# Performance work log

Hardware: AMD Instinct MI355X
Metric: run time of the kernel (lower is better)

The kernel has to match this reference:

```python
import jax, jax.numpy as jnp
import numpy as np

N, G, C, H, S = 16384, 100, 10, 32, 10  # batch, nb_genes, nb_chrom, hidden, signature
BN_EPS = 1e-5
SLOPE = 0.2


def setup_inputs() -> dict:
    key = jax.random.key(0)
    k = jax.random.split(key, 7)
    x = jax.random.randint(k[0], (N, G), 0, 3)                      # categorical genotype per gene
    emb = jax.random.normal(k[1], (G, 3, H), dtype=jnp.float32)      # per-gene entity embedding tables
    gene_att = jax.random.normal(k[2], (C, H), dtype=jnp.float32)    # GeneAttentionLayer attention matrix
    chrom_att = jax.random.normal(k[3], (1, H), dtype=jnp.float32)   # ChromAttentionLayer attention vector
    W = jax.random.normal(k[4], (H, S), dtype=jnp.float32) * 0.1     # linear layer weight
    b = jnp.zeros((S,), dtype=jnp.float32)                           # linear layer bias
    bn_gamma = jnp.ones((S,), dtype=jnp.float32)
    bn_beta = jnp.zeros((S,), dtype=jnp.float32)
    return {"x": x, "emb": emb, "gene_att": gene_att, "chrom_att": chrom_att,
            "W": W, "b": b, "bn_gamma": bn_gamma, "bn_beta": bn_beta}


def reference(x, emb, gene_att, chrom_att, W, b, bn_gamma, bn_beta):
    nb_genes, nb_chrom, hid = emb.shape[0], gene_att.shape[0], emb.shape[2]
    genes_per_chrom = nb_genes // nb_chrom
    # chrom composition matrix: comp[i, j] = 1 iff gene j belongs to chromosome i (contiguous blocks)
    comp = (jnp.arange(nb_genes) // genes_per_chrom == jnp.arange(nb_chrom)[:, None]).astype(emb.dtype)

    # --- entity embedding: h[n, g] = emb[g, x[n, g]]  -> (N, G, H)
    h = emb[jnp.arange(nb_genes)[None, :], x]

    # --- GeneAttentionLayer (avoids the dense (N, C, G, H) intermediate of the torch code)
    att = jnp.einsum('ch,ngh->ncg', gene_att, h) * comp[None]        # (N, C, G)
    mask = (att != 0).astype(h.dtype)                                # matches att.bool().byte()
    a = jnp.exp(jax.nn.leaky_relu(att, SLOPE)) * mask
    a = a / jnp.maximum(a.sum(axis=2, keepdims=True), 1e-10)
    chrom = jnp.einsum('ncg,ngh->nch', a, h)                         # (N, C, H) chromosome embeddings
    chrom = jax.nn.relu(chrom)                                       # dropout p=0 -> identity

    # --- ChromAttentionLayer
    catt = jnp.einsum('h,nch->nc', chrom_att[0], chrom)              # (N, C)
    ca = jnp.exp(jax.nn.leaky_relu(catt, SLOPE))
    ca = ca / ca.sum(axis=1, keepdims=True)
    g = jnp.einsum('nc,nch->nh', ca, chrom)                          # (N, H)
    g = jax.nn.relu(g)

    # --- linear + batch norm (training-mode batch statistics, biased variance as in torch BN)
    y = g @ W + b                                                    # (N, S)
    mu = y.mean(axis=0)
    var = ((y - mu) ** 2).mean(axis=0)
    return (y - mu) / jnp.sqrt(var + BN_EPS) * bn_gamma + bn_beta
```

## Files before the change

### kernel.cpp

```cpp
#include <hip/hip_runtime.h>
#include <hip/hip_fp16.h>

#define NROWS 16384
#define NG 100
#define NC 10
#define NH 32
#define NS 10
#define GPC 10
#define SLOPE 0.2f
#define BN_EPS 1e-5f

#define EPADH 36
#define RPB 32
#define BLOCK_A 512
#define NB (NROWS / RPB)


template<bool SLOTS>
__global__ __launch_bounds__(BLOCK_A, 4) void gga_main(
    const int* __restrict__ x, const float* __restrict__ emb,
    const float* __restrict__ gene_att, const float* __restrict__ chrom_att,
    const float* __restrict__ W, const float* __restrict__ b,
    float* __restrict__ y, float* __restrict__ P)
{
    __shared__ __half embL[300 * EPADH];
    __shared__ float eL[300];
    __shared__ float WTL[NS * NH];
    __shared__ float bL[NS];
    __shared__ unsigned xpL[RPB * 8];
    __shared__ float sAcc[2 * NS];

    const int t = threadIdx.x;
    const int n0 = blockIdx.x * RPB;

    for (int i = t; i < 2400; i += BLOCK_A) {
        float4 v = reinterpret_cast<const float4*>(emb)[i];
        int f = i << 2;
        int row = f >> 5, h = f & 31;
        __half2 lo = __floats2half2_rn(v.x, v.y);
        __half2 hi = __floats2half2_rn(v.z, v.w);
        uint2 u;
        u.x = __builtin_bit_cast(unsigned, lo);
        u.y = __builtin_bit_cast(unsigned, hi);
        *reinterpret_cast<uint2*>(&embL[row * EPADH + h]) = u;
    }
    for (int i = t; i < NH * NS; i += BLOCK_A) {
        int s = i >> 5, h = i & 31;
        WTL[i] = W[h * NS + s];
    }
    if (t < NS) bL[t] = b[t];
    if (t < 2 * NS) sAcc[t] = 0.f;
    if (t < 300) {
        const int g = t / 3;
        const float* ga = gene_att + (g / GPC) * NH;
        const float* e = emb + t * NH;
        float s = 0.f;
#pragma unroll
        for (int k = 0; k < NH; k += 4) {
            float4 ev = *reinterpret_cast<const float4*>(e + k);
            float4 gv = *reinterpret_cast<const float4*>(ga + k);
            s = fmaf(gv.x, ev.x, s); s = fmaf(gv.y, ev.y, s);
            s = fmaf(gv.z, ev.z, s); s = fmaf(gv.w, ev.w, s);
        }
        const float lk = s > 0.f ? s : SLOPE * s;
        eL[t] = (s != 0.f) ? __expf(lk) : 0.f;
    }
    if (t < 256) {
        const int r = t >> 3, w = t & 7;
        unsigned pw = 0u;
        if (w < 7) {
            const int4* p = reinterpret_cast<const int4*>(x + (n0 + r) * NG + w * 16);
            const int nv = (w < 6) ? 4 : 1;
#pragma unroll
            for (int i = 0; i < 4; ++i) {
                if (i < nv) {
                    int4 v = p[i];
                    pw |= ((unsigned)v.x & 3u) << (i * 8 + 0);
                    pw |= ((unsigned)v.y & 3u) << (i * 8 + 2);
                    pw |= ((unsigned)v.z & 3u) << (i * 8 + 4);
                    pw |= ((unsigned)v.w & 3u) << (i * 8 + 6);
                }
            }
        }
        xpL[r * 8 + w] = pw;
    }
    __syncthreads();

    const int lr = t >> 4;
    const int o = t & 15;
    const int n = n0 + lr;

    const float2 ca = reinterpret_cast<const float2*>(chrom_att)[o];

    const uint4 pa = *reinterpret_cast<const uint4*>(&xpL[lr * 8]);
    const uint4 pb = *reinterpret_cast<const uint4*>(&xpL[lr * 8 + 4]);
    const unsigned pk[8] = {pa.x, pa.y, pa.z, pa.w, pb.x, pb.y, pb.z, pb.w};

    float2 num = {0.f, 0.f};
    float den = 0.f;

#pragma unroll
    for (int c = 0; c < NC; ++c) {
        float e[GPC];
        float2 hf[GPC];
#pragma unroll
        for (int gp = 0; gp < GPC; ++gp) {
            const int g = c * GPC + gp;
            const unsigned xg = (pk[g >> 4] >> ((g & 15) * 2)) & 3u;
            const int r3 = g * 3 + (int)xg;
            e[gp] = eL[r3];
            __half2 hh = *reinterpret_cast<const __half2*>(&embL[r3 * EPADH + o * 2]);
            hf[gp] = __half22float2(hh);
        }
        float suma = 0.f;
#pragma unroll
        for (int gp = 0; gp < GPC; ++gp) suma += e[gp];
        const float inv = 1.f / fmaxf(suma, 1e-10f);

        float2 ch = {0.f, 0.f};
#pragma unroll
        for (int gp = 0; gp < GPC; ++gp) {
            ch.x = fmaf(e[gp], hf[gp].x, ch.x);
            ch.y = fmaf(e[gp], hf[gp].y, ch.y);
        }
        ch.x = fmaxf(ch.x, 0.f);
        ch.y = fmaxf(ch.y, 0.f);

        float pc = ch.x * ca.x + ch.y * ca.y;
        pc += __shfl_xor(pc, 1);
        pc += __shfl_xor(pc, 2);
        pc += __shfl_xor(pc, 4);
        pc += __shfl_xor(pc, 8);
        pc *= inv;
        const float lc = pc > 0.f ? pc : SLOPE * pc;
        const float ec = __expf(lc);
        const float w = ec * inv;

        num.x = fmaf(w, ch.x, num.x);
        num.y = fmaf(w, ch.y, num.y);
        den += ec;
    }

    const float invd = 1.f / den;
    const float g0 = fmaxf(num.x * invd, 0.f);
    const float g1 = fmaxf(num.y * invd, 0.f);

    float ys[NS];
#pragma unroll
    for (int s = 0; s < NS; ++s) {
        const float2 wv = *reinterpret_cast<const float2*>(&WTL[s * NH + o * 2]);
        float p = g0 * wv.x + g1 * wv.y;
        p += __shfl_xor(p, 1);
        p += __shfl_xor(p, 2);
        p += __shfl_xor(p, 4);
        p += __shfl_xor(p, 8);
        ys[s] = p + bL[s];
    }

    if (o == 0) {
        float2* yp = reinterpret_cast<float2*>(y + n * NS);
#pragma unroll
        for (int s2 = 0; s2 < 5; ++s2) yp[s2] = make_float2(ys[2 * s2], ys[2 * s2 + 1]);
    }

#pragma unroll
    for (int s = 0; s < NS; ++s) {
        float v = ys[s];
        float v2 = ys[s] * ys[s];
        v += __shfl_xor(v, 16);  v2 += __shfl_xor(v2, 16);
        v += __shfl_xor(v, 32);  v2 += __shfl_xor(v2, 32);
        if ((t & 63) == 0) {
            atomicAdd(&sAcc[s], v);
            atomicAdd(&sAcc[NS + s], v2);
        }
    }
    __syncthreads();
    if (t < 2 * NS) {
        if (SLOTS) P[t * NB + blockIdx.x] = sAcc[t];
        else       atomicAdd(&P[t], sAcc[t]);
    }
}

template<bool SLOTS>
__global__ __launch_bounds__(256) void gga_bn(
    float* __restrict__ out, const float* __restrict__ P,
    const float* __restrict__ gamma, const float* __restrict__ beta)
{
    __shared__ float red[2 * NS * 8];
    __shared__ float scL[NS], shL[NS];
    const int t = threadIdx.x;

    if (SLOTS) {
        if (t < 2 * NS * 8) {
            const int k = t >> 3, c = t & 7;
            const float4* p4 = reinterpret_cast<const float4*>(P + k * NB + c * 64);
            float s = 0.f;
#pragma unroll
            for (int i = 0; i < 16; ++i) {
                float4 v = p4[i];
                s += v.x + v.y + v.z + v.w;
            }
            red[t] = s;
        }
        __syncthreads();
    }
    if (t < NS) {
        float sm, sq;
        if (SLOTS) {
            sm = 0.f; sq = 0.f;
#pragma unroll
            for (int c = 0; c < 8; ++c) {
                sm += red[t * 8 + c];
                sq += red[(NS + t) * 8 + c];
            }
        } else {
            sm = P[t]; sq = P[NS + t];
        }
        const float mu = sm * (1.f / NROWS);
        float var = sq * (1.f / NROWS) - mu * mu;
        var = fmaxf(var, 0.f);
        const float r = rsqrtf(var + BN_EPS);
        scL[t] = gamma[t] * r;
        shL[t] = beta[t] - mu * scL[t];
    }
    __syncthreads();

    const int i4 = (blockIdx.x * 256 + t) * 4;
    float4 v = *reinterpret_cast<const float4*>(out + i4);
    const int s0 = i4 % NS;
    const int s1 = (s0 + 1) % NS, s2 = (s0 + 2) % NS, s3 = (s0 + 3) % NS;
    v.x = fmaf(v.x, scL[s0], shL[s0]);
    v.y = fmaf(v.y, scL[s1], shL[s1]);
    v.z = fmaf(v.z, scL[s2], shL[s2]);
    v.w = fmaf(v.w, scL[s3], shL[s3]);
    *reinterpret_cast<float4*>(out + i4) = v;
}

extern "C" void kernel_launch(void* const* d_in, const int* in_sizes, int n_in,
                              void* d_out, int out_size, void* d_ws, size_t ws_size,
                              hipStream_t stream) {
    const int*   x         = (const int*)d_in[0];
    const float* emb       = (const float*)d_in[1];
    const float* gene_att  = (const float*)d_in[2];
    const float* chrom_att = (const float*)d_in[3];
    const float* W         = (const float*)d_in[4];
    const float* b         = (const float*)d_in[5];
    const float* bn_gamma  = (const float*)d_in[6];
    const float* bn_beta   = (const float*)d_in[7];

    float* y = (float*)d_out;
    float* P = (float*)d_ws;

    if (ws_size >= (size_t)(2 * NS * NB * sizeof(float))) {
        gga_main<true><<<NB, BLOCK_A, 0, stream>>>(
            x, emb, gene_att, chrom_att, W, b, y, P);
        gga_bn<true><<<(NROWS * NS) / (256 * 4), 256, 0, stream>>>(
            y, P, bn_gamma, bn_beta);
    } else {
        hipMemsetAsync(P, 0, 2 * NS * sizeof(float), stream);
        gga_main<false><<<NB, BLOCK_A, 0, stream>>>(
            x, emb, gene_att, chrom_att, W, b, y, P);
        gga_bn<false><<<(NROWS * NS) / (256 * 4), 256, 0, stream>>>(
            y, P, bn_gamma, bn_beta);
    }
}
```

Before: 26.52 us.

## Halve threads per row, use DPP reductions, stripe global BN stat atomics

Each row is now handled by 8 lanes instead of 16, each lane covering 4 hidden dims with 64-bit LDS loads, and the block size drops to 256. Cross-lane sums use DPP row operations instead of ds_swizzle/shuffles. The per-block partial-sum slots and shared-memory atomics are replaced by global atomics spread over 8 stripes, with a memset before launch, which simplifies the BN kernel's reduction. The trade-offs are more global atomic contention and an extra memset launch, in exchange for fewer reduction instructions and less per-block overhead.

```diff
diff --git a/kernel.cpp b/kernel.cpp
--- a/kernel.cpp
+++ b/kernel.cpp
@@ -12,12 +12,23 @@
 
 #define EPADH 36
 #define RPB 32
-#define BLOCK_A 512
+#define BLOCK_A 256
 #define NB (NROWS / RPB)
 
-
-template<bool SLOTS>
-__global__ __launch_bounds__(BLOCK_A, 4) void gga_main(
+template<int CTRL>
+__device__ __forceinline__ float dpp_add(float v) {
+    int x = __builtin_bit_cast(int, v);
+    int y = __builtin_amdgcn_update_dpp(0, x, CTRL, 0xF, 0xF, true);
+    return v + __builtin_bit_cast(float, y);
+}
+__device__ __forceinline__ float row8_allreduce(float v) {
+    v = dpp_add<0xB1>(v);
+    v = dpp_add<0x4E>(v);
+    v = dpp_add<0x141>(v);
+    return v;
+}
+
+__global__ __launch_bounds__(BLOCK_A, 2) void gga_main(
     const int* __restrict__ x, const float* __restrict__ emb,
     const float* __restrict__ gene_att, const float* __restrict__ chrom_att,
     const float* __restrict__ W, const float* __restrict__ b,
@@ -28,7 +39,6 @@
     __shared__ float WTL[NS * NH];
     __shared__ float bL[NS];
     __shared__ unsigned xpL[RPB * 8];
-    __shared__ float sAcc[2 * NS];
 
     const int t = threadIdx.x;
     const int n0 = blockIdx.x * RPB;
@@ -49,11 +59,10 @@
         WTL[i] = W[h * NS + s];
     }
     if (t < NS) bL[t] = b[t];
-    if (t < 2 * NS) sAcc[t] = 0.f;
-    if (t < 300) {
-        const int g = t / 3;
+    for (int i = t; i < 300; i += BLOCK_A) {
+        const int g = i / 3;
         const float* ga = gene_att + (g / GPC) * NH;
-        const float* e = emb + t * NH;
+        const float* e = emb + i * NH;
         float s = 0.f;
 #pragma unroll
         for (int k = 0; k < NH; k += 4) {
@@ -63,9 +72,9 @@
             s = fmaf(gv.z, ev.z, s); s = fmaf(gv.w, ev.w, s);
         }
         const float lk = s > 0.f ? s : SLOPE * s;
-        eL[t] = (s != 0.f) ? __expf(lk) : 0.f;
-    }
-    if (t < 256) {
+        eL[i] = (s != 0.f) ? __expf(lk) : 0.f;
+    }
+    {
         const int r = t >> 3, w = t & 7;
         unsigned pw = 0u;
         if (w < 7) {
@@ -86,74 +95,73 @@
     }
     __syncthreads();
 
-    const int lr = t >> 4;
-    const int o = t & 15;
+    const int lr = t >> 3;
+    const int o = t & 7;
     const int n = n0 + lr;
 
-    const float2 ca = reinterpret_cast<const float2*>(chrom_att)[o];
+    const float4 ca = reinterpret_cast<const float4*>(chrom_att)[o];
 
     const uint4 pa = *reinterpret_cast<const uint4*>(&xpL[lr * 8]);
     const uint4 pb = *reinterpret_cast<const uint4*>(&xpL[lr * 8 + 4]);
     const unsigned pk[8] = {pa.x, pa.y, pa.z, pa.w, pb.x, pb.y, pb.z, pb.w};
 
-    float2 num = {0.f, 0.f};
+    float4 num = {0.f, 0.f, 0.f, 0.f};
     float den = 0.f;
 
 #pragma unroll
     for (int c = 0; c < NC; ++c) {
         float e[GPC];
-        float2 hf[GPC];
+        uint2 hu[GPC];
 #pragma unroll
         for (int gp = 0; gp < GPC; ++gp) {
             const int g = c * GPC + gp;
             const unsigned xg = (pk[g >> 4] >> ((g & 15) * 2)) & 3u;
             const int r3 = g * 3 + (int)xg;
             e[gp] = eL[r3];
-            __half2 hh = *reinterpret_cast<const __half2*>(&embL[r3 * EPADH + o * 2]);
-            hf[gp] = __half22float2(hh);
+            hu[gp] = *reinterpret_cast<const uint2*>(&embL[r3 * EPADH + o * 4]);
         }
         float suma = 0.f;
 #pragma unroll
         for (int gp = 0; gp < GPC; ++gp) suma += e[gp];
         const float inv = 1.f / fmaxf(suma, 1e-10f);
 
-        float2 ch = {0.f, 0.f};
+        float4 ch = {0.f, 0.f, 0.f, 0.f};
 #pragma unroll
         for (int gp = 0; gp < GPC; ++gp) {
-            ch.x = fmaf(e[gp], hf[gp].x, ch.x);
-            ch.y = fmaf(e[gp], hf[gp].y, ch.y);
-        }
-        ch.x = fmaxf(ch.x, 0.f);
-        ch.y = fmaxf(ch.y, 0.f);
-
-        float pc = ch.x * ca.x + ch.y * ca.y;
-        pc += __shfl_xor(pc, 1);
-        pc += __shfl_xor(pc, 2);
-        pc += __shfl_xor(pc, 4);
-        pc += __shfl_xor(pc, 8);
+            float2 a = __half22float2(__builtin_bit_cast(__half2, hu[gp].x));
+            float2 d = __half22float2(__builtin_bit_cast(__half2, hu[gp].y));
+            ch.x = fmaf(e[gp], a.x, ch.x);
+            ch.y = fmaf(e[gp], a.y, ch.y);
+            ch.z = fmaf(e[gp], d.x, ch.z);
+            ch.w = fmaf(e[gp], d.y, ch.w);
+        }
+        ch.x = fmaxf(ch.x, 0.f); ch.y = fmaxf(ch.y, 0.f);
+        ch.z = fmaxf(ch.z, 0.f); ch.w = fmaxf(ch.w, 0.f);
+
+        float pc = ch.x * ca.x + ch.y * ca.y + ch.z * ca.z + ch.w * ca.w;
+        pc = row8_allreduce(pc);
         pc *= inv;
         const float lc = pc > 0.f ? pc : SLOPE * pc;
         const float ec = __expf(lc);
         const float w = ec * inv;
 
-        num.x = fmaf(w, ch.x, num.x);
-        num.y = fmaf(w, ch.y, num.y);
+        num.x = fmaf(w, ch.x, num.x); num.y = fmaf(w, ch.y, num.y);
+        num.z = fmaf(w, ch.z, num.z); num.w = fmaf(w, ch.w, num.w);
         den += ec;
     }
 
     const float invd = 1.f / den;
     const float g0 = fmaxf(num.x * invd, 0.f);
     const float g1 = fmaxf(num.y * invd, 0.f);
+    const float g2 = fmaxf(num.z * invd, 0.f);
+    const float g3 = fmaxf(num.w * invd, 0.f);
 
     float ys[NS];
 #pragma unroll
     for (int s = 0; s < NS; ++s) {
-        const float2 wv = *reinterpret_cast<const float2*>(&WTL[s * NH + o * 2]);
-        float p = g0 * wv.x + g1 * wv.y;
-        p += __shfl_xor(p, 1);
-        p += __shfl_xor(p, 2);
-        p += __shfl_xor(p, 4);
-        p += __shfl_xor(p, 8);
+        const float4 wv = *reinterpret_cast<const float4*>(&WTL[s * NH + o * 4]);
+        float p = g0 * wv.x + g1 * wv.y + g2 * wv.z + g3 * wv.w;
+        p = row8_allreduce(p);
         ys[s] = p + bL[s];
     }
 
@@ -163,58 +171,34 @@
         for (int s2 = 0; s2 < 5; ++s2) yp[s2] = make_float2(ys[2 * s2], ys[2 * s2 + 1]);
     }
 
+    const int kstripe = (int)(blockIdx.x & 7);
 #pragma unroll
     for (int s = 0; s < NS; ++s) {
-        float v = ys[s];
+        float v  = ys[s];
         float v2 = ys[s] * ys[s];
-        v += __shfl_xor(v, 16);  v2 += __shfl_xor(v2, 16);
-        v += __shfl_xor(v, 32);  v2 += __shfl_xor(v2, 32);
+        v  = dpp_add<0x128>(v);
+        v2 = dpp_add<0x128>(v2);
+        v  += __shfl_xor(v, 16);  v2 += __shfl_xor(v2, 16);
+        v  += __shfl_xor(v, 32);  v2 += __shfl_xor(v2, 32);
         if ((t & 63) == 0) {
-            atomicAdd(&sAcc[s], v);
-            atomicAdd(&sAcc[NS + s], v2);
-        }
-    }
-    __syncthreads();
-    if (t < 2 * NS) {
-        if (SLOTS) P[t * NB + blockIdx.x] = sAcc[t];
-        else       atomicAdd(&P[t], sAcc[t]);
-    }
-}
-
-template<bool SLOTS>
+            atomicAdd(&P[kstripe * 64 + s],      v);
+            atomicAdd(&P[kstripe * 64 + 32 + s], v2);
+        }
+    }
+}
+
 __global__ __launch_bounds__(256) void gga_bn(
     float* __restrict__ out, const float* __restrict__ P,
     const float* __restrict__ gamma, const float* __restrict__ beta)
 {
-    __shared__ float red[2 * NS * 8];
     __shared__ float scL[NS], shL[NS];
     const int t = threadIdx.x;
-
-    if (SLOTS) {
-        if (t < 2 * NS * 8) {
-            const int k = t >> 3, c = t & 7;
-            const float4* p4 = reinterpret_cast<const float4*>(P + k * NB + c * 64);
-            float s = 0.f;
-#pragma unroll
-            for (int i = 0; i < 16; ++i) {
-                float4 v = p4[i];
-                s += v.x + v.y + v.z + v.w;
-            }
-            red[t] = s;
-        }
-        __syncthreads();
-    }
     if (t < NS) {
-        float sm, sq;
-        if (SLOTS) {
-            sm = 0.f; sq = 0.f;
-#pragma unroll
-            for (int c = 0; c < 8; ++c) {
-                sm += red[t * 8 + c];
-                sq += red[(NS + t) * 8 + c];
-            }
-        } else {
-            sm = P[t]; sq = P[NS + t];
+        float sm = 0.f, sq = 0.f;
+#pragma unroll
+        for (int k = 0; k < 8; ++k) {
+            sm += P[k * 64 + t];
+            sq += P[k * 64 + 32 + t];
         }
         const float mu = sm * (1.f / NROWS);
         float var = sq * (1.f / NROWS) - mu * mu;
@@ -251,16 +235,9 @@
     float* y = (float*)d_out;
     float* P = (float*)d_ws;
 
-    if (ws_size >= (size_t)(2 * NS * NB * sizeof(float))) {
-        gga_main<true><<<NB, BLOCK_A, 0, stream>>>(
-            x, emb, gene_att, chrom_att, W, b, y, P);
-        gga_bn<true><<<(NROWS * NS) / (256 * 4), 256, 0, stream>>>(
-            y, P, bn_gamma, bn_beta);
-    } else {
-        hipMemsetAsync(P, 0, 2 * NS * sizeof(float), stream);
-        gga_main<false><<<NB, BLOCK_A, 0, stream>>>(
-            x, emb, gene_att, chrom_att, W, b, y, P);
-        gga_bn<false><<<(NROWS * NS) / (256 * 4), 256, 0, stream>>>(
-            y, P, bn_gamma, bn_beta);
-    }
-}
+    hipMemsetAsync(P, 0, 2048, stream);
+    gga_main<<<NB, BLOCK_A, 0, stream>>>(
+        x, emb, gene_att, chrom_att, W, b, y, P);
+    gga_bn<<<(NROWS * NS) / (256 * 4), 256, 0, stream>>>(
+        y, P, bn_gamma, bn_beta);
+}
```

Measured after the change: 54.62 us. 2.06x slower.
